# Optimization experiments

Measured on AMD Instinct MI355X. Metric: run time of the kernel, lower is better.

Reference implementation:

```python
import jax, jax.numpy as jnp
import numpy as np

VOCAB, EMB = 32000, 300
B, T, S = 64, 25, 50
NF = 100
FS = (3, 4, 5)
H = 256
OUT = 31


def setup_inputs() -> dict:
    key = jax.random.key(0)
    ks = jax.random.split(key, 12)
    inp = {}
    inp["dialogue"] = jax.random.randint(ks[0], (B, T, S), 0, VOCAB)
    inp["emb"] = jax.random.normal(ks[1], (VOCAB, EMB), jnp.float32) * 0.1
    for j, fs in enumerate(FS):
        inp[f"conv_w{fs}"] = jax.random.normal(ks[2 + j], (NF, 1, fs, EMB), jnp.float32) * (1.0 / np.sqrt(fs * EMB))
        inp[f"conv_b{fs}"] = jnp.zeros((NF,), jnp.float32)
    IN = NF * len(FS)
    sc = 1.0 / np.sqrt(H)
    inp["wih"] = jax.random.normal(ks[5], (4 * H, IN), jnp.float32) * sc
    inp["whh"] = jax.random.normal(ks[6], (4 * H, H), jnp.float32) * sc
    inp["bih"] = jnp.zeros((4 * H,), jnp.float32)
    inp["bhh"] = jnp.zeros((4 * H,), jnp.float32)
    inp["wih_r"] = jax.random.normal(ks[7], (4 * H, IN), jnp.float32) * sc
    inp["whh_r"] = jax.random.normal(ks[8], (4 * H, H), jnp.float32) * sc
    inp["bih_r"] = jnp.zeros((4 * H,), jnp.float32)
    inp["bhh_r"] = jnp.zeros((4 * H,), jnp.float32)
    inp["h2o_w"] = jax.random.normal(ks[9], (OUT, 2 * H), jnp.float32) * sc
    inp["h2o_b"] = jnp.zeros((OUT,), jnp.float32)
    return inp


def _cnn_embed(tokens, emb, conv_params):
    # tokens: [B,T,S] int -> per-utterance CNN features [B,T, NF*len(FS)]
    x = emb[tokens.reshape(-1, S)]           # [B*T, S, EMB] embedding lookup
    x = x[:, None, :, :]                      # NCHW: [B*T, 1, S, EMB]
    feats = []
    for (w, b) in conv_params:
        c = jax.lax.conv_general_dilated(
            x, w, (1, 1), 'VALID', dimension_numbers=('NCHW', 'OIHW', 'NCHW'))
        c = jax.nn.relu(c + b[None, :, None, None])   # [B*T, NF, S-fs+1, 1]
        feats.append(jnp.max(c[..., 0], axis=2))      # max-pool over time -> [B*T, NF]
    return jnp.concatenate(feats, axis=1).reshape(B, T, -1)


def _lstm(x, wih, whh, bih, bhh):
    # single-layer LSTM, torch gate order (i, f, g, o); x: [B,Tm,I] -> [B,Tm,H]
    h0 = jnp.zeros((x.shape[0], H), x.dtype)

    def step(carry, xt):
        h, c = carry
        g = xt @ wih.T + h @ whh.T + bih + bhh        # [B, 4H]
        i, f, gg, o = jnp.split(g, 4, axis=-1)
        c = jax.nn.sigmoid(f) * c + jax.nn.sigmoid(i) * jnp.tanh(gg)
        h = jax.nn.sigmoid(o) * jnp.tanh(c)
        return (h, c), h

    _, hs = jax.lax.scan(step, (h0, h0), jnp.swapaxes(x, 0, 1))
    return jnp.swapaxes(hs, 0, 1)


def reference(dialogue, emb, conv_w3, conv_b3, conv_w4, conv_b4, conv_w5, conv_b5,
              wih, whh, bih, bhh, wih_r, whh_r, bih_r, bhh_r, h2o_w, h2o_b):
    r_in = _cnn_embed(dialogue, emb,
                      [(conv_w3, conv_b3), (conv_w4, conv_b4), (conv_w5, conv_b5)])
    # bi=True branch: self.rnn consumes the sequence in reverse order, outputs
    # stored back at their original positions == reverse, scan, reverse.
    rev = _lstm(r_in[:, ::-1], wih, whh, bih, bhh)[:, ::-1]
    # rnn_r consumes the sequence forward (teacher_forcing_ratio=None path)
    fwd = _lstm(r_in, wih_r, whh_r, bih_r, bhh_r)
    h = jnp.concatenate([rev, fwd], axis=-1)          # [B,T,2H]
    return jax.nn.sigmoid(h @ h2o_w.T + h2o_b)        # [B,T,OUT]
```

## Files before the change

### kernel.cpp

```cpp
#include <hip/hip_runtime.h>
#include <hip/hip_bf16.h>

#define NB 64
#define NT 25
#define NS 50
#define EMBD 300
#define NFILT 100
#define HD 256
#define NOUT 31
#define NBT (NB*NT)

#define KP3 928
#define KP4 1216
#define KP5 1504
#define XS_LEN 15104

typedef __attribute__((ext_vector_type(8))) short short8;
typedef __attribute__((ext_vector_type(4))) float f32x4;

__device__ __forceinline__ float hsum4(float4 a) { return (a.x + a.y) + (a.z + a.w); }
__device__ __forceinline__ void fma4(float4& a, float4 w, float4 x) {
    a.x = fmaf(w.x, x.x, a.x); a.y = fmaf(w.y, x.y, a.y);
    a.z = fmaf(w.z, x.z, a.z); a.w = fmaf(w.w, x.w, a.w);
}
__device__ __forceinline__ float sigmoidf_(float x) { return 1.0f / (1.0f + __expf(-x)); }
__device__ __forceinline__ float tanh_fast(float x) {
    x = fminf(fmaxf(x, -15.0f), 15.0f);
    const float e = __expf(2.0f * x);
    return (e - 1.0f) / (e + 1.0f);
}

__device__ __forceinline__ unsigned short f2bf(float f) {
    union { float f; unsigned u; } v; v.f = f;
    unsigned r = v.u + 0x7FFF + ((v.u >> 16) & 1);
    return (unsigned short)(r >> 16);
}

__device__ __forceinline__ short8 ld8_a8(const unsigned short* p) {
    short8 r;
    ((uint2*)&r)[0] = *(const uint2*)p;
    ((uint2*)&r)[1] = *(const uint2*)(p + 4);
    return r;
}

__global__ __launch_bounds__(256) void k_prep(
    const float* __restrict__ w3, const float* __restrict__ w4, const float* __restrict__ w5,
    unsigned short* __restrict__ wb)
{
    const int S0 = 112 * KP3, S1 = S0 + 112 * KP4, S2 = S1 + 112 * KP5;
    int idx = blockIdx.x * 256 + threadIdx.x;
    if (idx >= S2) return;
    int rel, Kp, K; const float* src;
    if (idx < S0)      { rel = idx;      Kp = KP3; K = 900;  src = w3; }
    else if (idx < S1) { rel = idx - S0; Kp = KP4; K = 1200; src = w4; }
    else               { rel = idx - S1; Kp = KP5; K = 1500; src = w5; }
    int f = rel / Kp, k = rel - f * Kp;
    float v = (f < NFILT && k < K) ? src[(size_t)f * K + k] : 0.0f;
    wb[idx] = f2bf(v);
}

__global__ __launch_bounds__(256) void k_prep2(
    const float* __restrict__ whh, const float* __restrict__ whh_r,
    unsigned short* __restrict__ wb2)
{
    const int idx = blockIdx.x * 256 + threadIdx.x;
    const int dir = idx >> 18;
    const int rem = idx & 262143;
    const int n = rem >> 8, k = rem & 255;
    const int j = n >> 2, gate = n & 3;
    const float* src = dir ? whh_r : whh;
    wb2[idx] = f2bf(src[(size_t)(gate * 256 + j) * 256 + k]);
}

__global__ __launch_bounds__(256) void k_conv(
    const int* __restrict__ tok, const float* __restrict__ emb,
    const unsigned short* __restrict__ wb,
    const float* __restrict__ b3, const float* __restrict__ b4, const float* __restrict__ b5,
    float* __restrict__ rin)
{
    __shared__ unsigned short xs[XS_LEN];
    const int bt = blockIdx.x;
    const int tid = threadIdx.x;
    const int* tk = tok + bt * NS;
    for (int i4 = tid; i4 < NS * (EMBD / 4); i4 += 256) {
        const int s = i4 / 75, e4 = i4 - s * 75;
        float4 v = ((const float4*)(emb + (size_t)tk[s] * EMBD))[e4];
        uint2 pk;
        pk.x = (unsigned)f2bf(v.x) | ((unsigned)f2bf(v.y) << 16);
        pk.y = (unsigned)f2bf(v.z) | ((unsigned)f2bf(v.w) << 16);
        *(uint2*)(xs + s * 300 + e4 * 4) = pk;
    }
    for (int i = NS * EMBD + tid; i < XS_LEN; i += 256) xs[i] = 0;
    __syncthreads();

    const int wave = tid >> 6, lane = tid & 63;
    const int col = lane & 15, kg = lane >> 4;

    for (int job = wave; job < 21; job += 4) {
        const int fsi = job / 7, ntile = job - fsi * 7;
        int Kp, P, obase; const unsigned short* W; const float* bias;
        if (fsi == 0)      { Kp = KP3; P = 48; W = wb;                       bias = b3; obase = 0; }
        else if (fsi == 1) { Kp = KP4; P = 47; W = wb + 112 * KP3;           bias = b4; obase = NFILT; }
        else               { Kp = KP5; P = 46; W = wb + 112 * (KP3 + KP4);   bias = b5; obase = 2 * NFILT; }

        const unsigned short* wrow = W + (size_t)(ntile * 16 + col) * Kp + kg * 8;
        const unsigned short* xbase = xs + (size_t)(lane & 15) * 300 + kg * 8;
        f32x4 acc0 = {0,0,0,0}, acc1 = {0,0,0,0}, acc2 = {0,0,0,0};

        const int nks = Kp / 32;
        for (int ks = 0; ks < nks; ++ks) {
            const int k0 = ks * 32;
            short8 bfrag = *(const short8*)(wrow + k0);
            short8 a0 = ld8_a8(xbase + k0);
            short8 a1 = ld8_a8(xbase + 16 * 300 + k0);
            short8 a2 = ld8_a8(xbase + 32 * 300 + k0);
            acc0 = __builtin_amdgcn_mfma_f32_16x16x32_bf16(a0, bfrag, acc0, 0, 0, 0);
            acc1 = __builtin_amdgcn_mfma_f32_16x16x32_bf16(a1, bfrag, acc1, 0, 0, 0);
            acc2 = __builtin_amdgcn_mfma_f32_16x16x32_bf16(a2, bfrag, acc2, 0, 0, 0);
        }

        float pmax = -1e30f;
        #pragma unroll
        for (int reg = 0; reg < 4; ++reg) {
            pmax = fmaxf(pmax, acc0[reg]);
            pmax = fmaxf(pmax, acc1[reg]);
            const int r2 = 32 + kg * 4 + reg;
            if (r2 < P) pmax = fmaxf(pmax, acc2[reg]);
        }
        pmax = fmaxf(pmax, __shfl_xor(pmax, 16, 64));
        pmax = fmaxf(pmax, __shfl_xor(pmax, 32, 64));
        if (lane < 16) {
            const int f = ntile * 16 + lane;
            if (f < NFILT)
                rin[(size_t)bt * (3 * NFILT) + obase + f] = fmaxf(0.0f, pmax + bias[f]);
        }
    }
}

__global__ __launch_bounds__(256) void k_gin(
    const float* __restrict__ rin,
    const float* __restrict__ wih,   const float* __restrict__ bih,   const float* __restrict__ bhh,
    const float* __restrict__ wih_r, const float* __restrict__ bih_r, const float* __restrict__ bhh_r,
    float* __restrict__ gin)
{
    __shared__ float xsh[8 * EMBD];
    const int bt0 = blockIdx.x * 8;
    const int tid = threadIdx.x;
    const float4* src = (const float4*)(rin + (size_t)bt0 * EMBD);
    for (int i4 = tid; i4 < 8 * EMBD / 4; i4 += 256) ((float4*)xsh)[i4] = src[i4];
    __syncthreads();
    for (int g2 = tid; g2 < 2 * 1024; g2 += 256) {
        const int d = g2 >> 10;
        const int g = g2 & 1023;
        const float* wp = (d ? wih_r : wih) + (size_t)g * EMBD;
        const float bb = d ? (bih_r[g] + bhh_r[g]) : (bih[g] + bhh[g]);
        const float4* w4p = (const float4*)wp;
        float4 acc[8];
        #pragma unroll
        for (int r = 0; r < 8; ++r) acc[r] = {0,0,0,0};
        for (int k = 0; k < EMBD / 4; ++k) {
            const float4 wv = w4p[k];
            #pragma unroll
            for (int r = 0; r < 8; ++r) fma4(acc[r], wv, ((const float4*)(xsh + r * EMBD))[k]);
        }
        const int gp = ((g & 255) << 2) | (g >> 8);
        #pragma unroll
        for (int r = 0; r < 8; ++r)
            gin[((size_t)d * NBT + bt0 + r) * 1024 + gp] = hsum4(acc[r]) + bb;
    }
}

__global__ __launch_bounds__(256, 1) void k_lstm(
    const float* __restrict__ gin, const unsigned short* __restrict__ wb2,
    float* __restrict__ hglob, unsigned* __restrict__ cnt,
    float* __restrict__ hs)
{
    const int bid = blockIdx.x;
    const int dir = bid >> 2, ow = bid & 3;
    const int tid = threadIdx.x;
    const int wave = tid >> 6, lane = tid & 63;
    const int l15 = lane & 15, kg = lane >> 4;

    __shared__ unsigned short h_lds[64 * 264];
    __shared__ float slab[4][1280];

    const unsigned short* wbase = wb2 + (size_t)dir * (1024 * 256);
    short8 barr[4][8];
#pragma unroll
    for (int nt = 0; nt < 4; ++nt) {
        const int ng = ow * 256 + wave * 64 + nt * 16 + l15;
#pragma unroll
        for (int kk = 0; kk < 8; ++kk)
            barr[nt][kk] = *(const short8*)(wbase + (size_t)ng * 256 + kk * 32 + kg * 8);
    }

    float c[4][4];
#pragma unroll
    for (int mt = 0; mt < 4; ++mt)
#pragma unroll
        for (int q = 0; q < 4; ++q) c[mt][q] = 0.0f;

    float* hg = hglob + (size_t)dir * (2 * 64 * 256);
    unsigned* mycnt = cnt + dir * 64;
    const float* ginb = gin + (size_t)dir * NBT * 1024;
    float* hsb = hs + (size_t)dir * NBT * HD;

    for (int s = 0; s < NT; ++s) {
        const int t = dir ? s : (NT - 1 - s);
        const float* hcur = hg + (s & 1) * (64 * 256);
        float* hnext = hg + ((s + 1) & 1) * (64 * 256);

#pragma unroll
        for (int r = 0; r < 16; ++r) {
            const int i4 = tid + 256 * r;
            const int b = i4 >> 6, k4 = i4 & 63;
            float4 v = ((const float4*)hcur)[i4];
            uint2 pk;
            pk.x = (unsigned)f2bf(v.x) | ((unsigned)f2bf(v.y) << 16);
            pk.y = (unsigned)f2bf(v.z) | ((unsigned)f2bf(v.w) << 16);
            *(uint2*)(h_lds + b * 264 + k4 * 4) = pk;
        }
        __syncthreads();

        f32x4 acc[4][4];
#pragma unroll
        for (int mt = 0; mt < 4; ++mt)
#pragma unroll
            for (int nt = 0; nt < 4; ++nt) acc[mt][nt] = (f32x4){0.f, 0.f, 0.f, 0.f};

#pragma unroll
        for (int kk = 0; kk < 8; ++kk) {
            short8 a[4];
#pragma unroll
            for (int mt = 0; mt < 4; ++mt)
                a[mt] = *(const short8*)(h_lds + (mt * 16 + l15) * 264 + kk * 32 + kg * 8);
#pragma unroll
            for (int mt = 0; mt < 4; ++mt)
#pragma unroll
                for (int nt = 0; nt < 4; ++nt)
                    acc[mt][nt] = __builtin_amdgcn_mfma_f32_16x16x32_bf16(a[mt], barr[nt][kk], acc[mt][nt], 0, 0, 0);
        }

#pragma unroll
        for (int mt = 0; mt < 4; ++mt) {
#pragma unroll
            for (int nt = 0; nt < 4; ++nt)
                *(f32x4*)(&slab[wave][(nt * 16 + l15) * 20 + kg * 4]) = acc[mt][nt];
#pragma unroll
            for (int q = 0; q < 4; ++q) {
                const int j = q * 4 + kg;
                const int jg = ow * 64 + wave * 16 + j;
                const int bg = mt * 16 + l15;
                const float gI = slab[wave][(j * 4 + 0) * 20 + l15];
                const float gF = slab[wave][(j * 4 + 1) * 20 + l15];
                const float gG = slab[wave][(j * 4 + 2) * 20 + l15];
                const float gO = slab[wave][(j * 4 + 3) * 20 + l15];
                const float4 gx = *(const float4*)(ginb + (size_t)(bg * NT + t) * 1024 + jg * 4);
                const float vi = sigmoidf_(gI + gx.x);
                const float vf = sigmoidf_(gF + gx.y);
                const float vg = tanh_fast(gG + gx.z);
                const float vo = sigmoidf_(gO + gx.w);
                const float cc = vf * c[mt][q] + vi * vg;
                c[mt][q] = cc;
                const float hh = vo * tanh_fast(cc);
                hnext[bg * 256 + jg] = hh;
                hsb[(size_t)(bg * NT + t) * HD + jg] = hh;
            }
        }

        __threadfence();
        __syncthreads();
        if (tid == 0) {
            atomicAdd(mycnt, 1u);
            const unsigned target = 4u * (unsigned)(s + 1);
            while (atomicAdd(mycnt, 0u) < target) __builtin_amdgcn_s_sleep(8);
        }
        __syncthreads();
        __threadfence();
    }
}

__global__ __launch_bounds__(64) void k_out(
    const float* __restrict__ hs, const float* __restrict__ w, const float* __restrict__ bias,
    float* __restrict__ out)
{
    __shared__ float hsh[2 * HD];
    const int bt = blockIdx.x;
    const int tid = threadIdx.x;
    const float4* rev4 = (const float4*)(hs + (size_t)bt * HD);
    const float4* fwd4 = (const float4*)(hs + ((size_t)NBT + bt) * HD);
    for (int i = tid; i < 2 * HD / 4; i += 64)
        ((float4*)hsh)[i] = (i < HD / 4) ? rev4[i] : fwd4[i - HD / 4];
    __syncthreads();
    if (tid < NOUT) {
        const float4* wr = (const float4*)(w + (size_t)tid * (2 * HD));
        float4 acc{0,0,0,0};
        for (int k = 0; k < 2 * HD / 4; ++k) fma4(acc, wr[k], ((const float4*)hsh)[k]);
        out[(size_t)bt * NOUT + tid] = sigmoidf_(hsum4(acc) + bias[tid]);
    }
}

extern "C" void kernel_launch(void* const* d_in, const int* in_sizes, int n_in,
                              void* d_out, int out_size, void* d_ws, size_t ws_size,
                              hipStream_t stream)
{
    const int*   tok   = (const int*)d_in[0];
    const float* emb   = (const float*)d_in[1];
    const float* w3    = (const float*)d_in[2];
    const float* b3    = (const float*)d_in[3];
    const float* w4    = (const float*)d_in[4];
    const float* b4    = (const float*)d_in[5];
    const float* w5    = (const float*)d_in[6];
    const float* b5    = (const float*)d_in[7];
    const float* wih   = (const float*)d_in[8];
    const float* whh   = (const float*)d_in[9];
    const float* bih   = (const float*)d_in[10];
    const float* bhh   = (const float*)d_in[11];
    const float* wih_r = (const float*)d_in[12];
    const float* whh_r = (const float*)d_in[13];
    const float* bih_r = (const float*)d_in[14];
    const float* bhh_r = (const float*)d_in[15];
    const float* h2o_w = (const float*)d_in[16];
    const float* h2o_b = (const float*)d_in[17];

    float* ws  = (float*)d_ws;
    float* rin = ws;
    float* gin = rin + (size_t)NBT * 3 * NFILT;
    float* hs  = gin + (size_t)2 * NBT * 1024;
    unsigned short* wb = (unsigned short*)gin;
    unsigned short* wb2   = (unsigned short*)rin;
    float*          hglob = rin + 262144;
    unsigned*       cnt   = (unsigned*)(rin + 262144 + 65536);

    k_prep <<<1596, 256, 0, stream>>>(w3, w4, w5, wb);
    k_conv <<<NBT, 256, 0, stream>>>(tok, emb, wb, b3, b4, b5, rin);
    k_gin  <<<NBT / 8, 256, 0, stream>>>(rin, wih, bih, bhh, wih_r, bih_r, bhh_r, gin);
    hipMemsetAsync(hglob, 0, (65536 + 128) * sizeof(float), stream);
    k_prep2<<<2048, 256, 0, stream>>>(whh, whh_r, wb2);
    k_lstm <<<8, 256, 0, stream>>>(gin, wb2, hglob, cnt, hs);
    k_out  <<<NBT, 64, 0, stream>>>(hs, h2o_w, h2o_b, (float*)d_out);
}
```

Before: 587.6 us.

## Split LSTM by batch per block to drop grid sync; two samples per conv block

The LSTM kernel now splits work across blocks by batch quarter instead of by gate columns. Each 512-thread block owns 16 batch rows and the full hidden state, so the per-step global atomic barrier and global h exchange go away. h lives in double-buffered LDS as bf16. Recurrent weights are now streamed from global/L2 every step instead of held in registers. The gate-input layout is changed to [t][b] so per-step reads are contiguous, and the conv kernel handles two utterances per block so each weight fragment is reused across both.

Measured after the change: 789.5 us. 34.4% more time.

```diff
diff --git a/kernel.cpp b/kernel.cpp
--- a/kernel.cpp
+++ b/kernel.cpp
@@ -78,19 +78,21 @@
     const float* __restrict__ b3, const float* __restrict__ b4, const float* __restrict__ b5,
     float* __restrict__ rin)
 {
-    __shared__ unsigned short xs[XS_LEN];
-    const int bt = blockIdx.x;
+    __shared__ unsigned short xs[2][XS_LEN];
+    const int bt0 = blockIdx.x * 2;
     const int tid = threadIdx.x;
-    const int* tk = tok + bt * NS;
-    for (int i4 = tid; i4 < NS * (EMBD / 4); i4 += 256) {
-        const int s = i4 / 75, e4 = i4 - s * 75;
-        float4 v = ((const float4*)(emb + (size_t)tk[s] * EMBD))[e4];
+    for (int i4 = tid; i4 < 2 * NS * 75; i4 += 256) {
+        const int smp = i4 / (NS * 75);
+        const int rem = i4 - smp * (NS * 75);
+        const int s = rem / 75, e4 = rem - s * 75;
+        const int t = tok[(bt0 + smp) * NS + s];
+        float4 v = ((const float4*)(emb + (size_t)t * EMBD))[e4];
         uint2 pk;
         pk.x = (unsigned)f2bf(v.x) | ((unsigned)f2bf(v.y) << 16);
         pk.y = (unsigned)f2bf(v.z) | ((unsigned)f2bf(v.w) << 16);
-        *(uint2*)(xs + s * 300 + e4 * 4) = pk;
-    }
-    for (int i = NS * EMBD + tid; i < XS_LEN; i += 256) xs[i] = 0;
+        *(uint2*)(&xs[smp][s * 300 + e4 * 4]) = pk;
+    }
+    for (int i = NS * EMBD + tid; i < XS_LEN; i += 256) { xs[0][i] = 0; xs[1][i] = 0; }
     __syncthreads();
 
     const int wave = tid >> 6, lane = tid & 63;
@@ -104,35 +106,48 @@
         else               { Kp = KP5; P = 46; W = wb + 112 * (KP3 + KP4);   bias = b5; obase = 2 * NFILT; }
 
         const unsigned short* wrow = W + (size_t)(ntile * 16 + col) * Kp + kg * 8;
-        const unsigned short* xbase = xs + (size_t)(lane & 15) * 300 + kg * 8;
-        f32x4 acc0 = {0,0,0,0}, acc1 = {0,0,0,0}, acc2 = {0,0,0,0};
+        const unsigned short* xb0 = &xs[0][col * 300 + kg * 8];
+        const unsigned short* xb1 = &xs[1][col * 300 + kg * 8];
+        f32x4 a00 = {0,0,0,0}, a01 = {0,0,0,0}, a02 = {0,0,0,0};
+        f32x4 a10 = {0,0,0,0}, a11 = {0,0,0,0}, a12 = {0,0,0,0};
 
         const int nks = Kp / 32;
         for (int ks = 0; ks < nks; ++ks) {
             const int k0 = ks * 32;
             short8 bfrag = *(const short8*)(wrow + k0);
-            short8 a0 = ld8_a8(xbase + k0);
-            short8 a1 = ld8_a8(xbase + 16 * 300 + k0);
-            short8 a2 = ld8_a8(xbase + 32 * 300 + k0);
-            acc0 = __builtin_amdgcn_mfma_f32_16x16x32_bf16(a0, bfrag, acc0, 0, 0, 0);
-            acc1 = __builtin_amdgcn_mfma_f32_16x16x32_bf16(a1, bfrag, acc1, 0, 0, 0);
-            acc2 = __builtin_amdgcn_mfma_f32_16x16x32_bf16(a2, bfrag, acc2, 0, 0, 0);
-        }
-
-        float pmax = -1e30f;
+            short8 p0 = ld8_a8(xb0 + k0);
+            short8 p1 = ld8_a8(xb0 + 16 * 300 + k0);
+            short8 p2 = ld8_a8(xb0 + 32 * 300 + k0);
+            short8 q0 = ld8_a8(xb1 + k0);
+            short8 q1 = ld8_a8(xb1 + 16 * 300 + k0);
+            short8 q2 = ld8_a8(xb1 + 32 * 300 + k0);
+            a00 = __builtin_amdgcn_mfma_f32_16x16x32_bf16(p0, bfrag, a00, 0, 0, 0);
+            a01 = __builtin_amdgcn_mfma_f32_16x16x32_bf16(p1, bfrag, a01, 0, 0, 0);
+            a02 = __builtin_amdgcn_mfma_f32_16x16x32_bf16(p2, bfrag, a02, 0, 0, 0);
+            a10 = __builtin_amdgcn_mfma_f32_16x16x32_bf16(q0, bfrag, a10, 0, 0, 0);
+            a11 = __builtin_amdgcn_mfma_f32_16x16x32_bf16(q1, bfrag, a11, 0, 0, 0);
+            a12 = __builtin_amdgcn_mfma_f32_16x16x32_bf16(q2, bfrag, a12, 0, 0, 0);
+        }
+
+        float pm0 = -1e30f, pm1 = -1e30f;
         #pragma unroll
         for (int reg = 0; reg < 4; ++reg) {
-            pmax = fmaxf(pmax, acc0[reg]);
-            pmax = fmaxf(pmax, acc1[reg]);
+            pm0 = fmaxf(pm0, a00[reg]); pm0 = fmaxf(pm0, a01[reg]);
+            pm1 = fmaxf(pm1, a10[reg]); pm1 = fmaxf(pm1, a11[reg]);
             const int r2 = 32 + kg * 4 + reg;
-            if (r2 < P) pmax = fmaxf(pmax, acc2[reg]);
-        }
-        pmax = fmaxf(pmax, __shfl_xor(pmax, 16, 64));
-        pmax = fmaxf(pmax, __shfl_xor(pmax, 32, 64));
+            if (r2 < P) { pm0 = fmaxf(pm0, a02[reg]); pm1 = fmaxf(pm1, a12[reg]); }
+        }
+        pm0 = fmaxf(pm0, __shfl_xor(pm0, 16, 64));
+        pm0 = fmaxf(pm0, __shfl_xor(pm0, 32, 64));
+        pm1 = fmaxf(pm1, __shfl_xor(pm1, 16, 64));
+        pm1 = fmaxf(pm1, __shfl_xor(pm1, 32, 64));
         if (lane < 16) {
             const int f = ntile * 16 + lane;
-            if (f < NFILT)
-                rin[(size_t)bt * (3 * NFILT) + obase + f] = fmaxf(0.0f, pmax + bias[f]);
+            if (f < NFILT) {
+                const float bb = bias[f];
+                rin[(size_t)bt0 * (3 * NFILT) + obase + f]       = fmaxf(0.0f, pm0 + bb);
+                rin[(size_t)(bt0 + 1) * (3 * NFILT) + obase + f] = fmaxf(0.0f, pm1 + bb);
+            }
         }
     }
 }
@@ -165,118 +180,90 @@
         }
         const int gp = ((g & 255) << 2) | (g >> 8);
         #pragma unroll
-        for (int r = 0; r < 8; ++r)
-            gin[((size_t)d * NBT + bt0 + r) * 1024 + gp] = hsum4(acc[r]) + bb;
-    }
-}
-
-__global__ __launch_bounds__(256, 1) void k_lstm(
-    const float* __restrict__ gin, const unsigned short* __restrict__ wb2,
-    float* __restrict__ hglob, unsigned* __restrict__ cnt,
+        for (int r = 0; r < 8; ++r) {
+            const int bt = bt0 + r;
+            const int b = bt / NT, t = bt - b * NT;
+            gin[(((size_t)d * NT + t) * NB + b) * 1024 + gp] = hsum4(acc[r]) + bb;
+        }
+    }
+}
+
+__global__ __launch_bounds__(512, 1) void k_lstm(
+    const float* __restrict__ gin,
+    const unsigned short* __restrict__ wb2,
     float* __restrict__ hs)
 {
     const int bid = blockIdx.x;
-    const int dir = bid >> 2, ow = bid & 3;
+    const int dir = bid >> 2, bq = bid & 3;
     const int tid = threadIdx.x;
     const int wave = tid >> 6, lane = tid & 63;
     const int l15 = lane & 15, kg = lane >> 4;
 
-    __shared__ unsigned short h_lds[64 * 264];
-    __shared__ float slab[4][1280];
-
-    const unsigned short* wbase = wb2 + (size_t)dir * (1024 * 256);
-    short8 barr[4][8];
-#pragma unroll
-    for (int nt = 0; nt < 4; ++nt) {
-        const int ng = ow * 256 + wave * 64 + nt * 16 + l15;
-#pragma unroll
-        for (int kk = 0; kk < 8; ++kk)
-            barr[nt][kk] = *(const short8*)(wbase + (size_t)ng * 256 + kk * 32 + kg * 8);
-    }
-
-    float c[4][4];
-#pragma unroll
-    for (int mt = 0; mt < 4; ++mt)
-#pragma unroll
-        for (int q = 0; q < 4; ++q) c[mt][q] = 0.0f;
-
-    float* hg = hglob + (size_t)dir * (2 * 64 * 256);
-    unsigned* mycnt = cnt + dir * 64;
-    const float* ginb = gin + (size_t)dir * NBT * 1024;
+    __shared__ unsigned short hb[2][16 * 264];
+    __shared__ float slab[8][32 * 20];
+
+    for (int i = tid; i < 16 * 264; i += 512) hb[0][i] = 0;
+    __syncthreads();
+
+    const unsigned short* wb_w = wb2 + (size_t)dir * (1024 * 256)
+                               + (size_t)(wave * 128 + l15) * 256 + kg * 8;
+    const float* gb = gin + (size_t)dir * (NT * NB * 1024);
     float* hsb = hs + (size_t)dir * NBT * HD;
+
+    float c[8];
+    #pragma unroll
+    for (int q = 0; q < 8; ++q) c[q] = 0.0f;
+
+    const int j_local = lane & 7;
+    const int b_lo = (lane >> 3) & 7;
 
     for (int s = 0; s < NT; ++s) {
         const int t = dir ? s : (NT - 1 - s);
-        const float* hcur = hg + (s & 1) * (64 * 256);
-        float* hnext = hg + ((s + 1) & 1) * (64 * 256);
-
-#pragma unroll
-        for (int r = 0; r < 16; ++r) {
-            const int i4 = tid + 256 * r;
-            const int b = i4 >> 6, k4 = i4 & 63;
-            float4 v = ((const float4*)hcur)[i4];
-            uint2 pk;
-            pk.x = (unsigned)f2bf(v.x) | ((unsigned)f2bf(v.y) << 16);
-            pk.y = (unsigned)f2bf(v.z) | ((unsigned)f2bf(v.w) << 16);
-            *(uint2*)(h_lds + b * 264 + k4 * 4) = pk;
-        }
-        __syncthreads();
-
-        f32x4 acc[4][4];
-#pragma unroll
-        for (int mt = 0; mt < 4; ++mt)
-#pragma unroll
-            for (int nt = 0; nt < 4; ++nt) acc[mt][nt] = (f32x4){0.f, 0.f, 0.f, 0.f};
-
-#pragma unroll
+        const unsigned short* hc = hb[s & 1];
+        unsigned short* hn = hb[(s + 1) & 1];
+
+        f32x4 acc[8];
+        #pragma unroll
+        for (int nt = 0; nt < 8; ++nt) acc[nt] = (f32x4){0.f, 0.f, 0.f, 0.f};
+
+        #pragma unroll 2
         for (int kk = 0; kk < 8; ++kk) {
-            short8 a[4];
-#pragma unroll
-            for (int mt = 0; mt < 4; ++mt)
-                a[mt] = *(const short8*)(h_lds + (mt * 16 + l15) * 264 + kk * 32 + kg * 8);
-#pragma unroll
-            for (int mt = 0; mt < 4; ++mt)
-#pragma unroll
-                for (int nt = 0; nt < 4; ++nt)
-                    acc[mt][nt] = __builtin_amdgcn_mfma_f32_16x16x32_bf16(a[mt], barr[nt][kk], acc[mt][nt], 0, 0, 0);
-        }
-
-#pragma unroll
-        for (int mt = 0; mt < 4; ++mt) {
-#pragma unroll
-            for (int nt = 0; nt < 4; ++nt)
-                *(f32x4*)(&slab[wave][(nt * 16 + l15) * 20 + kg * 4]) = acc[mt][nt];
-#pragma unroll
-            for (int q = 0; q < 4; ++q) {
-                const int j = q * 4 + kg;
-                const int jg = ow * 64 + wave * 16 + j;
-                const int bg = mt * 16 + l15;
-                const float gI = slab[wave][(j * 4 + 0) * 20 + l15];
-                const float gF = slab[wave][(j * 4 + 1) * 20 + l15];
-                const float gG = slab[wave][(j * 4 + 2) * 20 + l15];
-                const float gO = slab[wave][(j * 4 + 3) * 20 + l15];
-                const float4 gx = *(const float4*)(ginb + (size_t)(bg * NT + t) * 1024 + jg * 4);
+            short8 av = *(const short8*)(hc + l15 * 264 + kk * 32 + kg * 8);
+            #pragma unroll
+            for (int nt = 0; nt < 8; ++nt) {
+                short8 bb = *(const short8*)(wb_w + nt * (16 * 256) + kk * 32);
+                acc[nt] = __builtin_amdgcn_mfma_f32_16x16x32_bf16(av, bb, acc[nt], 0, 0, 0);
+            }
+        }
+
+        float* sw = &slab[wave][0];
+        #pragma unroll
+        for (int ntp = 0; ntp < 4; ++ntp) {
+            *(f32x4*)(sw + l15 * 20 + kg * 4)        = acc[2 * ntp];
+            *(f32x4*)(sw + (16 + l15) * 20 + kg * 4) = acc[2 * ntp + 1];
+            #pragma unroll
+            for (int p = 0; p < 2; ++p) {
+                const int b_row = b_lo + p * 8;
+                const int bglob = bq * 16 + b_row;
+                const int j_g = wave * 32 + ntp * 8 + j_local;
+                const float gI = sw[(j_local * 4 + 0) * 20 + b_row];
+                const float gF = sw[(j_local * 4 + 1) * 20 + b_row];
+                const float gG = sw[(j_local * 4 + 2) * 20 + b_row];
+                const float gO = sw[(j_local * 4 + 3) * 20 + b_row];
+                const float4 gx = *(const float4*)(gb + (((size_t)t * NB + bglob) << 10) + j_g * 4);
                 const float vi = sigmoidf_(gI + gx.x);
                 const float vf = sigmoidf_(gF + gx.y);
                 const float vg = tanh_fast(gG + gx.z);
                 const float vo = sigmoidf_(gO + gx.w);
-                const float cc = vf * c[mt][q] + vi * vg;
-                c[mt][q] = cc;
+                const int ci = ntp * 2 + p;
+                const float cc = vf * c[ci] + vi * vg;
+                c[ci] = cc;
                 const float hh = vo * tanh_fast(cc);
-                hnext[bg * 256 + jg] = hh;
-                hsb[(size_t)(bg * NT + t) * HD + jg] = hh;
+                hn[b_row * 264 + j_g] = f2bf(hh);
+                hsb[((size_t)bglob * NT + t) * HD + j_g] = hh;
             }
         }
-
-        __threadfence();
         __syncthreads();
-        if (tid == 0) {
-            atomicAdd(mycnt, 1u);
-            const unsigned target = 4u * (unsigned)(s + 1);
-            while (atomicAdd(mycnt, 0u) < target) __builtin_amdgcn_s_sleep(8);
-        }
-        __syncthreads();
-        __threadfence();
     }
 }
 
@@ -328,15 +315,12 @@
     float* gin = rin + (size_t)NBT * 3 * NFILT;
     float* hs  = gin + (size_t)2 * NBT * 1024;
     unsigned short* wb = (unsigned short*)gin;
-    unsigned short* wb2   = (unsigned short*)rin;
-    float*          hglob = rin + 262144;
-    unsigned*       cnt   = (unsigned*)(rin + 262144 + 65536);
+    unsigned short* wb2 = (unsigned short*)rin;
 
     k_prep <<<1596, 256, 0, stream>>>(w3, w4, w5, wb);
-    k_conv <<<NBT, 256, 0, stream>>>(tok, emb, wb, b3, b4, b5, rin);
+    k_conv <<<NBT / 2, 256, 0, stream>>>(tok, emb, wb, b3, b4, b5, rin);
     k_gin  <<<NBT / 8, 256, 0, stream>>>(rin, wih, bih, bhh, wih_r, bih_r, bhh_r, gin);
-    hipMemsetAsync(hglob, 0, (65536 + 128) * sizeof(float), stream);
     k_prep2<<<2048, 256, 0, stream>>>(whh, whh_r, wb2);
-    k_lstm <<<8, 256, 0, stream>>>(gin, wb2, hglob, cnt, hs);
+    k_lstm <<<8, 512, 0, stream>>>(gin, wb2, hs);
     k_out  <<<NBT, 64, 0, stream>>>(hs, h2o_w, h2o_b, (float*)d_out);
 }
```
